# Optimization experiments

Hardware: AMD Instinct MI355X
Metric: run time of the kernel (lower is better)

Reference implementation:

```python
import jax, jax.numpy as jnp
import numpy as np

B, T, N, C = 2, 12, 4096, 32
FILTERS = [32, 32, 32]


def setup_inputs() -> dict:
    key = jax.random.key(0)
    ks = jax.random.split(key, 12)
    inp = {
        'data': jax.random.normal(ks[0], (B, T, N, C), dtype=jnp.float32),
        'adj': jax.random.uniform(ks[1], (3 * N, 3 * N), dtype=jnp.float32) / (3.0 * N),
        'temporal_emb': jax.random.normal(ks[2], (1, T, 1, C), dtype=jnp.float32) * 0.0003,
        'spatial_emb': jax.random.normal(ks[3], (1, 1, N, C), dtype=jnp.float32) * 0.0003,
    }
    c_in = C
    for i, f in enumerate(FILTERS):
        scale = 1.0 / np.sqrt(c_in)
        inp[f'W{i}'] = jax.random.uniform(ks[4 + 2 * i], (c_in, 2 * f), dtype=jnp.float32,
                                          minval=-scale, maxval=scale)
        inp[f'b{i}'] = jnp.zeros((2 * f,), dtype=jnp.float32)
        c_in = f
    return inp


def reference(data, adj, temporal_emb, spatial_emb, W0, b0, W1, b1, W2, b2):
    # data: (B, T, N, C). Add temporal + spatial position embeddings.
    x = data + temporal_emb + spatial_emb
    b, t, n, c = x.shape
    w = t - 2  # number of sliding windows
    # Gather all 3-step windows at once: (B, W, 3, N, C) -> (B, W, 3N, C)
    idx = jnp.arange(w)[:, None] + jnp.arange(3)[None, :]
    xw = x[:, idx].reshape(b, w, 3 * n, c)
    outs = []
    for Wl, bl in ((W0, b0), (W1, b1), (W2, b2)):
        # dense graph conv over the 3N local graph, batched over (B, W)
        xw = jnp.einsum('nm,bwmc->bwnc', adj, xw)
        y = xw @ Wl + bl            # (B, W, 3N, 2*C')
        lhs, rhs = jnp.split(y, 2, axis=-1)
        xw = lhs * jax.nn.sigmoid(rhs)  # GLU, (B, W, 3N, C')
        outs.append(xw[:, :, n:2 * n, :])  # crop middle timestep
    # stacked max over the gcn layers: (B, T-2, N, C_last)
    return jnp.max(jnp.stack(outs, axis=0), axis=0)
```

## Files before the change

kernel.cpp:

```cpp
#include <hip/hip_runtime.h>

#define NN 4096
#define TT 12
#define BB 2
#define CC 32
#define WW 10
#define K3 12288
#define NCOL 640
#define SA 4096.0f
#define SX 1024.0f
#define BM 48
#define BNH 320
#define BK 32
#define NT (K3 / BK)

typedef _Float16 half8 __attribute__((ext_vector_type(8)));
typedef _Float16 half4_t __attribute__((ext_vector_type(4)));
typedef float floatx4 __attribute__((ext_vector_type(4)));

__global__ void k_conv_adj(const float* __restrict__ adj, _Float16* __restrict__ a16) {
    long n4 = (long)K3 * K3 / 4;
    long i = (long)blockIdx.x * blockDim.x + threadIdx.x;
    long stride = (long)gridDim.x * blockDim.x;
    const float4* src = (const float4*)adj;
    half4_t* dst = (half4_t*)a16;
    for (; i < n4; i += stride) {
        float4 v = src[i];
        half4_t h;
        h[0] = (_Float16)(v.x * SA);
        h[1] = (_Float16)(v.y * SA);
        h[2] = (_Float16)(v.z * SA);
        h[3] = (_Float16)(v.w * SA);
        dst[i] = h;
    }
}

__global__ void k_prep(const float* __restrict__ data, const float* __restrict__ temb,
                       const float* __restrict__ semb, _Float16* __restrict__ x0t) {
    __shared__ float sb[CC][64 + 1];
    int z = blockIdx.y;
    int b = z / 30; int r = z % 30; int w = r / 3; int j = r % 3;
    int t = w + j;
    int n0 = blockIdx.x * 64;
    int tid = threadIdx.x;
    for (int e = tid; e < 64 * CC; e += 256) {
        int nl = e >> 5, c = e & 31;
        float v = data[((long)(b * TT + t) * NN + n0 + nl) * CC + c]
                + temb[t * CC + c] + semb[(n0 + nl) * CC + c];
        sb[c][nl] = v;
    }
    __syncthreads();
    int bw = b * WW + w;
    for (int e = tid; e < 64 * CC; e += 256) {
        int c = e >> 6, nl = e & 63;
        x0t[(long)(bw * CC + c) * K3 + j * NN + n0 + nl] = (_Float16)sb[c][nl];
    }
}

__device__ __forceinline__ void gload_lds16(const _Float16* g, _Float16* l) {
    __builtin_amdgcn_global_load_lds(
        (const __attribute__((address_space(1))) void*)g,
        (__attribute__((address_space(3))) void*)l, 16, 0, 0);
}

template <int MODE>
__global__ __launch_bounds__(256, 2) void k_gemm_glu(
    const _Float16* __restrict__ A, const _Float16* __restrict__ BT,
    const float* __restrict__ Wt, const float* __restrict__ bias,
    _Float16* __restrict__ outH,
    const _Float16* __restrict__ x1, const _Float16* __restrict__ x2,
    float* __restrict__ outF,
    float invS, int Mvalid)
{
    __shared__ __attribute__((aligned(16))) _Float16 AB[3][11776];
    __shared__ float WB[CC * 64 + 64];

    int tid = threadIdx.x;
    int lane = tid & 63, wid = tid >> 6;

    int nblk = gridDim.x;
    int q = nblk >> 3, r = nblk & 7;
    int xcd = blockIdx.x & 7, idx = blockIdx.x >> 3;
    int lin = (xcd < r ? xcd * (q + 1) : r * (q + 1) + (xcd - r) * q) + idx;
    int mt = lin >> 1, nh = lin & 1;
    long m0 = (long)mt * BM;
    int n0 = nh * BNH;

    for (int e = tid; e < CC * 64; e += 256) WB[e] = Wt[e];
    if (tid < 64) WB[CC * 64 + tid] = bias[tid];

    int rowA = tid >> 2, kbA_st = tid & 3;
    int ksA = kbA_st ^ ((rowA >> 1) & 3);
    const _Float16* aS = A + (m0 + rowA) * (long)K3 + ksA * 8;
    const _Float16* bS[5];
#pragma unroll
    for (int i = 0; i < 5; ++i) {
        int ci = i * 256 + tid;
        int row = ci >> 2, kb = ci & 3;
        int ks = kb ^ ((row >> 1) & 3);
        bS[i] = BT + (long)(n0 + row) * K3 + ks * 8;
    }

#define STAGE(bufi, kOff)                                                   \
    do {                                                                    \
        _Float16* bp = &AB[bufi][0];                                        \
        gload_lds16(bS[0] + (kOff), bp + 1536 + (0 * 256 + wid * 64) * 8);  \
        gload_lds16(bS[1] + (kOff), bp + 1536 + (1 * 256 + wid * 64) * 8);  \
        gload_lds16(bS[2] + (kOff), bp + 1536 + (2 * 256 + wid * 64) * 8);  \
        gload_lds16(bS[3] + (kOff), bp + 1536 + (3 * 256 + wid * 64) * 8);  \
        gload_lds16(bS[4] + (kOff), bp + 1536 + (4 * 256 + wid * 64) * 8);  \
        if (wid < 3) gload_lds16(aS + (kOff), bp + wid * 512);              \
    } while (0)

    int fr = lane & 15, kq = lane >> 4;
    int kbs = kq ^ ((fr >> 1) & 3);
    int aOff[3], bOff[5];
#pragma unroll
    for (int ms = 0; ms < 3; ++ms) aOff[ms] = (ms * 16 + fr) * 32 + kbs * 8;
#pragma unroll
    for (int ns = 0; ns < 5; ++ns) bOff[ns] = 1536 + (wid * 80 + ns * 16 + fr) * 32 + kbs * 8;

    floatx4 acc[3][5] = {};

    STAGE(0, 0);
    STAGE(1, BK);
    STAGE(2, 2 * BK);

    int cur = 0;
#pragma unroll 1
    for (int t = 0; t < NT; ++t) {
        int ahead = NT - 1 - t;
        if (wid < 3) {
            if (ahead >= 2)      asm volatile("s_waitcnt vmcnt(12)" ::: "memory");
            else if (ahead == 1) asm volatile("s_waitcnt vmcnt(6)" ::: "memory");
            else                 asm volatile("s_waitcnt vmcnt(0)" ::: "memory");
        } else {
            if (ahead >= 2)      asm volatile("s_waitcnt vmcnt(10)" ::: "memory");
            else if (ahead == 1) asm volatile("s_waitcnt vmcnt(5)" ::: "memory");
            else                 asm volatile("s_waitcnt vmcnt(0)" ::: "memory");
        }
        __builtin_amdgcn_s_barrier();

        const _Float16* P = &AB[cur][0];
        half8 af[3], bf[5];
#pragma unroll
        for (int ms = 0; ms < 3; ++ms) af[ms] = *(const half8*)(P + aOff[ms]);
#pragma unroll
        for (int ns = 0; ns < 5; ++ns) bf[ns] = *(const half8*)(P + bOff[ns]);

        asm volatile("s_waitcnt lgkmcnt(0)" ::: "memory");
        __builtin_amdgcn_sched_barrier(0);
        __builtin_amdgcn_s_barrier();

        if (t + 3 < NT) { STAGE(cur, (long)(t + 3) * BK); }
        __builtin_amdgcn_sched_barrier(0);

#pragma unroll
        for (int ms = 0; ms < 3; ++ms)
#pragma unroll
            for (int ns = 0; ns < 5; ++ns)
                acc[ms][ns] = __builtin_amdgcn_mfma_f32_16x16x32_f16(af[ms], bf[ns], acc[ms][ns], 0, 0, 0);

        cur = (cur == 2) ? 0 : cur + 1;
    }
#undef STAGE

    float* scr = (float*)AB;
    const int SCRW = 321;
    int rb = (lane >> 4) * 4, cb = lane & 15;

    __syncthreads();
#pragma unroll
    for (int ms = 0; ms < 3; ++ms)
#pragma unroll
        for (int ns = 0; ns < 5; ++ns)
#pragma unroll
            for (int i = 0; i < 4; ++i)
                scr[(ms * 16 + rb + i) * SCRW + wid * 80 + ns * 16 + cb] = acc[ms][ns][i];
    __syncthreads();

    for (int e = tid; e < 480; e += 256) {
        int row = e % 48;
        int bwl = e / 48;
        int bw = nh * 10 + bwl;
        long m = m0 + row;
        float g[CC];
#pragma unroll
        for (int c = 0; c < CC; ++c) g[c] = scr[row * SCRW + bwl * 32 + c] * invS;
        float y[64];
#pragma unroll
        for (int o = 0; o < 64; ++o) y[o] = WB[CC * 64 + o];
#pragma unroll
        for (int c = 0; c < CC; ++c) {
            float gv = g[c];
#pragma unroll
            for (int o = 0; o < 64; ++o) y[o] = fmaf(gv, WB[c * 64 + o], y[o]);
        }
        if (MODE == 0) {
#pragma unroll
            for (int c = 0; c < CC; ++c) {
                float rr = y[c] * (1.f / (1.f + __expf(-y[c + 32])));
                outH[(long)(bw * CC + c) * K3 + m] = (_Float16)(rr * SX);
            }
        } else {
            if (m < Mvalid) {
                float res[CC];
#pragma unroll
                for (int c = 0; c < CC; ++c) {
                    float rr = y[c] * (1.f / (1.f + __expf(-y[c + 32])));
                    float v1 = (float)x1[(long)(bw * CC + c) * K3 + NN + m] * (1.f / SX);
                    float v2 = (float)x2[(long)(bw * CC + c) * K3 + NN + m] * (1.f / SX);
                    res[c] = fmaxf(rr, fmaxf(v1, v2));
                }
                float4* op = (float4*)(outF + ((long)bw * NN + m) * CC);
#pragma unroll
                for (int qv = 0; qv < CC / 4; ++qv)
                    op[qv] = make_float4(res[qv * 4 + 0], res[qv * 4 + 1], res[qv * 4 + 2], res[qv * 4 + 3]);
            }
        }
    }
}

extern "C" void kernel_launch(void* const* d_in, const int* in_sizes, int n_in,
                              void* d_out, int out_size, void* d_ws, size_t ws_size,
                              hipStream_t stream)
{
    const float* data = (const float*)d_in[0];
    const float* adj  = (const float*)d_in[1];
    const float* temb = (const float*)d_in[2];
    const float* semb = (const float*)d_in[3];
    const float* W0 = (const float*)d_in[4];
    const float* b0 = (const float*)d_in[5];
    const float* W1 = (const float*)d_in[6];
    const float* b1 = (const float*)d_in[7];
    const float* W2 = (const float*)d_in[8];
    const float* b2 = (const float*)d_in[9];
    float* out = (float*)d_out;
    (void)ws_size; (void)in_sizes; (void)n_in; (void)out_size;

    char* ws = (char*)d_ws;
    _Float16* A16 = (_Float16*)ws;  ws += (size_t)K3 * K3 * 2;
    _Float16* X0  = (_Float16*)ws;  ws += (size_t)NCOL * K3 * 2;
    _Float16* X1  = (_Float16*)ws;  ws += (size_t)NCOL * K3 * 2;
    _Float16* X2  = (_Float16*)ws;  ws += (size_t)NCOL * K3 * 2;

    k_conv_adj<<<4096, 256, 0, stream>>>(adj, A16);
    k_prep<<<dim3(64, 60), 256, 0, stream>>>(data, temb, semb, X0);

    k_gemm_glu<0><<<512, 256, 0, stream>>>(A16, X0, W0, b0, X1,
                                           nullptr, nullptr, nullptr, 1.f / SA, K3);
    k_gemm_glu<0><<<512, 256, 0, stream>>>(A16, X1, W1, b1, X2,
                                           nullptr, nullptr, nullptr, 1.f / (SA * SX), K3);
    k_gemm_glu<1><<<172, 256, 0, stream>>>(A16 + (size_t)NN * K3, X2, W2, b2, nullptr,
                                           X1, X2, out, 1.f / (SA * SX), NN);
}
```

Baseline: 1.324 ms.

## Replace LDS-staged GEMM pipeline with direct global-to-register double buffering

After: 2.159 ms. 1.63x slower.

```diff
diff --git a/kernel.cpp b/kernel.cpp
--- a/kernel.cpp
+++ b/kernel.cpp
@@ -2,7 +2,6 @@
 
 #define NN 4096
 #define TT 12
-#define BB 2
 #define CC 32
 #define WW 10
 #define K3 12288
@@ -10,7 +9,6 @@
 #define SA 4096.0f
 #define SX 1024.0f
 #define BM 48
-#define BNH 320
 #define BK 32
 #define NT (K3 / BK)
 
@@ -57,12 +55,6 @@
     }
 }
 
-__device__ __forceinline__ void gload_lds16(const _Float16* g, _Float16* l) {
-    __builtin_amdgcn_global_load_lds(
-        (const __attribute__((address_space(1))) void*)g,
-        (__attribute__((address_space(3))) void*)l, 16, 0, 0);
-}
-
 template <int MODE>
 __global__ __launch_bounds__(256, 2) void k_gemm_glu(
     const _Float16* __restrict__ A, const _Float16* __restrict__ BT,
@@ -72,103 +64,92 @@
     float* __restrict__ outF,
     float invS, int Mvalid)
 {
-    __shared__ __attribute__((aligned(16))) _Float16 AB[3][11776];
+    __shared__ float scr[BM * 321];
     __shared__ float WB[CC * 64 + 64];
+    const int SCRW = 321;
 
     int tid = threadIdx.x;
     int lane = tid & 63, wid = tid >> 6;
 
     int nblk = gridDim.x;
     int q = nblk >> 3, r = nblk & 7;
-    int xcd = blockIdx.x & 7, idx = blockIdx.x >> 3;
-    int lin = (xcd < r ? xcd * (q + 1) : r * (q + 1) + (xcd - r) * q) + idx;
+    int xcd = blockIdx.x & 7, bi = blockIdx.x >> 3;
+    int lin = (xcd < r ? xcd * (q + 1) : r * (q + 1) + (xcd - r) * q) + bi;
     int mt = lin >> 1, nh = lin & 1;
     long m0 = (long)mt * BM;
-    int n0 = nh * BNH;
+    int n0 = nh * 320;
 
     for (int e = tid; e < CC * 64; e += 256) WB[e] = Wt[e];
     if (tid < 64) WB[CC * 64 + tid] = bias[tid];
 
-    int rowA = tid >> 2, kbA_st = tid & 3;
-    int ksA = kbA_st ^ ((rowA >> 1) & 3);
-    const _Float16* aS = A + (m0 + rowA) * (long)K3 + ksA * 8;
-    const _Float16* bS[5];
-#pragma unroll
-    for (int i = 0; i < 5; ++i) {
-        int ci = i * 256 + tid;
-        int row = ci >> 2, kb = ci & 3;
-        int ks = kb ^ ((row >> 1) & 3);
-        bS[i] = BT + (long)(n0 + row) * K3 + ks * 8;
-    }
-
-#define STAGE(bufi, kOff)                                                   \
-    do {                                                                    \
-        _Float16* bp = &AB[bufi][0];                                        \
-        gload_lds16(bS[0] + (kOff), bp + 1536 + (0 * 256 + wid * 64) * 8);  \
-        gload_lds16(bS[1] + (kOff), bp + 1536 + (1 * 256 + wid * 64) * 8);  \
-        gload_lds16(bS[2] + (kOff), bp + 1536 + (2 * 256 + wid * 64) * 8);  \
-        gload_lds16(bS[3] + (kOff), bp + 1536 + (3 * 256 + wid * 64) * 8);  \
-        gload_lds16(bS[4] + (kOff), bp + 1536 + (4 * 256 + wid * 64) * 8);  \
-        if (wid < 3) gload_lds16(aS + (kOff), bp + wid * 512);              \
+    int fr = lane & 15, kq = lane >> 4;
+
+    const _Float16* aP0 = A + (m0 +  0 + fr) * (long)K3 + kq * 8;
+    const _Float16* aP1 = A + (m0 + 16 + fr) * (long)K3 + kq * 8;
+    const _Float16* aP2 = A + (m0 + 32 + fr) * (long)K3 + kq * 8;
+    int cb0 = n0 + wid * 80 + fr;
+    const _Float16* bP0 = BT + (long)(cb0 +  0) * K3 + kq * 8;
+    const _Float16* bP1 = BT + (long)(cb0 + 16) * K3 + kq * 8;
+    const _Float16* bP2 = BT + (long)(cb0 + 32) * K3 + kq * 8;
+    const _Float16* bP3 = BT + (long)(cb0 + 48) * K3 + kq * 8;
+    const _Float16* bP4 = BT + (long)(cb0 + 64) * K3 + kq * 8;
+
+    floatx4 acc[3][5] = {};
+
+#define LOAD_SET(sa0, sa1, sa2, sb0, sb1, sb2, sb3, sb4, OFF)      \
+    do {                                                           \
+        sa0 = *(const half8*)(aP0 + (OFF));                        \
+        sa1 = *(const half8*)(aP1 + (OFF));                        \
+        sa2 = *(const half8*)(aP2 + (OFF));                        \
+        sb0 = *(const half8*)(bP0 + (OFF));                        \
+        sb1 = *(const half8*)(bP1 + (OFF));                        \
+        sb2 = *(const half8*)(bP2 + (OFF));                        \
+        sb3 = *(const half8*)(bP3 + (OFF));                        \
+        sb4 = *(const half8*)(bP4 + (OFF));                        \
     } while (0)
 
-    int fr = lane & 15, kq = lane >> 4;
-    int kbs = kq ^ ((fr >> 1) & 3);
-    int aOff[3], bOff[5];
-#pragma unroll
-    for (int ms = 0; ms < 3; ++ms) aOff[ms] = (ms * 16 + fr) * 32 + kbs * 8;
-#pragma unroll
-    for (int ns = 0; ns < 5; ++ns) bOff[ns] = 1536 + (wid * 80 + ns * 16 + fr) * 32 + kbs * 8;
-
-    floatx4 acc[3][5] = {};
-
-    STAGE(0, 0);
-    STAGE(1, BK);
-    STAGE(2, 2 * BK);
-
-    int cur = 0;
+#define MFMA_SET(sa0, sa1, sa2, sb0, sb1, sb2, sb3, sb4)                              \
+    do {                                                                              \
+        acc[0][0] = __builtin_amdgcn_mfma_f32_16x16x32_f16(sa0, sb0, acc[0][0],0,0,0);\
+        acc[0][1] = __builtin_amdgcn_mfma_f32_16x16x32_f16(sa0, sb1, acc[0][1],0,0,0);\
+        acc[0][2] = __builtin_amdgcn_mfma_f32_16x16x32_f16(sa0, sb2, acc[0][2],0,0,0);\
+        acc[0][3] = __builtin_amdgcn_mfma_f32_16x16x32_f16(sa0, sb3, acc[0][3],0,0,0);\
+        acc[0][4] = __builtin_amdgcn_mfma_f32_16x16x32_f16(sa0, sb4, acc[0][4],0,0,0);\
+        acc[1][0] = __builtin_amdgcn_mfma_f32_16x16x32_f16(sa1, sb0, acc[1][0],0,0,0);\
+        acc[1][1] = __builtin_amdgcn_mfma_f32_16x16x32_f16(sa1, sb1, acc[1][1],0,0,0);\
+        acc[1][2] = __builtin_amdgcn_mfma_f32_16x16x32_f16(sa1, sb2, acc[1][2],0,0,0);\
+        acc[1][3] = __builtin_amdgcn_mfma_f32_16x16x32_f16(sa1, sb3, acc[1][3],0,0,0);\
+        acc[1][4] = __builtin_amdgcn_mfma_f32_16x16x32_f16(sa1, sb4, acc[1][4],0,0,0);\
+        acc[2][0] = __builtin_amdgcn_mfma_f32_16x16x32_f16(sa2, sb0, acc[2][0],0,0,0);\
+        acc[2][1] = __builtin_amdgcn_mfma_f32_16x16x32_f16(sa2, sb1, acc[2][1],0,0,0);\
+        acc[2][2] = __builtin_amdgcn_mfma_f32_16x16x32_f16(sa2, sb2, acc[2][2],0,0,0);\
+        acc[2][3] = __builtin_amdgcn_mfma_f32_16x16x32_f16(sa2, sb3, acc[2][3],0,0,0);\
+        acc[2][4] = __builtin_amdgcn_mfma_f32_16x16x32_f16(sa2, sb4, acc[2][4],0,0,0);\
+    } while (0)
+
+    half8 aA0, aA1, aA2, bA0, bA1, bA2, bA3, bA4;
+    half8 aB0, aB1, aB2, bB0, bB1, bB2, bB3, bB4;
+
+    LOAD_SET(aA0, aA1, aA2, bA0, bA1, bA2, bA3, bA4, 0);
+    LOAD_SET(aB0, aB1, aB2, bB0, bB1, bB2, bB3, bB4, BK);
+    aP0 += 2 * BK; aP1 += 2 * BK; aP2 += 2 * BK;
+    bP0 += 2 * BK; bP1 += 2 * BK; bP2 += 2 * BK; bP3 += 2 * BK; bP4 += 2 * BK;
+
 #pragma unroll 1
-    for (int t = 0; t < NT; ++t) {
-        int ahead = NT - 1 - t;
-        if (wid < 3) {
-            if (ahead >= 2)      asm volatile("s_waitcnt vmcnt(12)" ::: "memory");
-            else if (ahead == 1) asm volatile("s_waitcnt vmcnt(6)" ::: "memory");
-            else                 asm volatile("s_waitcnt vmcnt(0)" ::: "memory");
-        } else {
-            if (ahead >= 2)      asm volatile("s_waitcnt vmcnt(10)" ::: "memory");
-            else if (ahead == 1) asm volatile("s_waitcnt vmcnt(5)" ::: "memory");
-            else                 asm volatile("s_waitcnt vmcnt(0)" ::: "memory");
-        }
-        __builtin_amdgcn_s_barrier();
-
-        const _Float16* P = &AB[cur][0];
-        half8 af[3], bf[5];
-#pragma unroll
-        for (int ms = 0; ms < 3; ++ms) af[ms] = *(const half8*)(P + aOff[ms]);
-#pragma unroll
-        for (int ns = 0; ns < 5; ++ns) bf[ns] = *(const half8*)(P + bOff[ns]);
-
-        asm volatile("s_waitcnt lgkmcnt(0)" ::: "memory");
-        __builtin_amdgcn_sched_barrier(0);
-        __builtin_amdgcn_s_barrier();
-
-        if (t + 3 < NT) { STAGE(cur, (long)(t + 3) * BK); }
-        __builtin_amdgcn_sched_barrier(0);
-
-#pragma unroll
-        for (int ms = 0; ms < 3; ++ms)
-#pragma unroll
-            for (int ns = 0; ns < 5; ++ns)
-                acc[ms][ns] = __builtin_amdgcn_mfma_f32_16x16x32_f16(af[ms], bf[ns], acc[ms][ns], 0, 0, 0);
-
-        cur = (cur == 2) ? 0 : cur + 1;
-    }
-#undef STAGE
-
-    float* scr = (float*)AB;
-    const int SCRW = 321;
+    for (int t = 0; t + 3 < NT; t += 2) {
+        MFMA_SET(aA0, aA1, aA2, bA0, bA1, bA2, bA3, bA4);
+        LOAD_SET(aA0, aA1, aA2, bA0, bA1, bA2, bA3, bA4, 0);
+        MFMA_SET(aB0, aB1, aB2, bB0, bB1, bB2, bB3, bB4);
+        LOAD_SET(aB0, aB1, aB2, bB0, bB1, bB2, bB3, bB4, BK);
+        aP0 += 2 * BK; aP1 += 2 * BK; aP2 += 2 * BK;
+        bP0 += 2 * BK; bP1 += 2 * BK; bP2 += 2 * BK; bP3 += 2 * BK; bP4 += 2 * BK;
+    }
+    MFMA_SET(aA0, aA1, aA2, bA0, bA1, bA2, bA3, bA4);
+    MFMA_SET(aB0, aB1, aB2, bB0, bB1, bB2, bB3, bB4);
+#undef LOAD_SET
+#undef MFMA_SET
+
     int rb = (lane >> 4) * 4, cb = lane & 15;
-
     __syncthreads();
 #pragma unroll
     for (int ms = 0; ms < 3; ++ms)
```
